# Performance work log

Hardware: AMD Instinct MI355X
Metric: run time of the kernel (lower is better)

Reference implementation:

```python
import jax, jax.numpy as jnp
import numpy as np

DIM = 1024
FF = 4096
E = 8
K = 2


def setup_inputs() -> dict:
    key = jax.random.key(0)
    ks = jax.random.split(key, 6)
    x = jax.random.normal(ks[0], (4, 2048, DIM), dtype=jnp.float32)
    wr = jax.random.normal(ks[1], (E, DIM), dtype=jnp.float32) * 0.02   # router weight [E, D]
    w1 = jax.random.normal(ks[2], (E, DIM, 2 * FF), dtype=jnp.float32) * 0.02  # SwiGLU in-proj
    b1 = jax.random.normal(ks[3], (E, 2 * FF), dtype=jnp.float32) * 0.02
    w2 = jax.random.normal(ks[4], (E, FF, DIM), dtype=jnp.float32) * 0.02  # SwiGLU out-proj
    b2 = jax.random.normal(ks[5], (E, DIM), dtype=jnp.float32) * 0.02
    return {"x": x, "wr": wr, "w1": w1, "b1": b1, "w2": w2, "b2": b2}


def reference(x, wr, w1, b1, w2, b2):
    B, T, D = x.shape
    n_experts = wr.shape[0]
    xf = x.reshape(B * T, D)                      # [N, D]
    logits = xf @ wr.T                            # [N, E]
    topk_vals, topk_idx = jax.lax.top_k(logits, K)  # [N, K]
    gates = jax.nn.softmax(topk_vals, axis=-1)      # [N, K]
    out = jnp.zeros_like(xf)
    for e in range(n_experts):
        # combined gate weight for tokens routed to expert e (0 otherwise)
        g_e = jnp.sum(jnp.where(topk_idx == e, gates, 0.0), axis=-1)  # [N]
        u = xf @ w1[e] + b1[e]                    # [N, 2F]
        a, b = jnp.split(u, 2, axis=-1)
        h = jax.nn.silu(a) * b                    # SwiGLU
        y_e = h @ w2[e] + b2[e]                   # [N, D]
        out = out + g_e[:, None] * y_e
    return out.reshape(B, T, D)
```

## Files before the change

### kernel.cpp

```cpp
#include <hip/hip_runtime.h>

#define NE 8
#define NTOK 8192
#define NDIM 1024
#define NFF 4096

typedef short bf16x8 __attribute__((ext_vector_type(8)));
typedef float f32x4 __attribute__((ext_vector_type(4)));
typedef unsigned short us_t;
typedef us_t us4 __attribute__((ext_vector_type(4)));

__device__ __forceinline__ us_t f2bf(float f) {
  unsigned int u = __float_as_uint(f);
  u += 0x7fffu + ((u >> 16) & 1u);
  return (us_t)(u >> 16);
}

__device__ __forceinline__ void gload16(const void* g, void* l) {
  __builtin_amdgcn_global_load_lds(
      (const __attribute__((address_space(1))) void*)g,
      (__attribute__((address_space(3))) void*)l, 16, 0, 0);
}

__global__ __launch_bounds__(256) void router_kernel(
    const float* __restrict__ x, const float* __restrict__ wr,
    int* __restrict__ counts, int* __restrict__ tok_list, float* __restrict__ gate_list,
    us_t* __restrict__ xbf)
{
  __shared__ float wr_s[NE * NDIM];
  int tid = threadIdx.x;
#pragma unroll
  for (int i = 0; i < 8; ++i)
    ((float4*)wr_s)[tid + 256 * i] = ((const float4*)wr)[tid + 256 * i];
  __syncthreads();
  int w = tid >> 6, l = tid & 63;
  int t = blockIdx.x * 4 + w;
  float4 xv[4];
#pragma unroll
  for (int j = 0; j < 4; ++j) xv[j] = ((const float4*)x)[(size_t)t * 256 + j * 64 + l];
#pragma unroll
  for (int j = 0; j < 4; ++j) {
    us4 o;
    o.x = f2bf(xv[j].x); o.y = f2bf(xv[j].y); o.z = f2bf(xv[j].z); o.w = f2bf(xv[j].w);
    ((us4*)xbf)[(size_t)t * 256 + j * 64 + l] = o;
  }
  float logits[NE];
#pragma unroll
  for (int e = 0; e < NE; ++e) {
    float p = 0.f;
#pragma unroll
    for (int j = 0; j < 4; ++j) {
      float4 wv = ((const float4*)wr_s)[e * 256 + j * 64 + l];
      p += xv[j].x * wv.x + xv[j].y * wv.y + xv[j].z * wv.z + xv[j].w * wv.w;
    }
#pragma unroll
    for (int s = 32; s > 0; s >>= 1) p += __shfl_xor(p, s, 64);
    logits[e] = p;
  }
  if (l == 0) {
    int e1 = 0; float v1 = logits[0];
#pragma unroll
    for (int e = 1; e < NE; ++e) if (logits[e] > v1) { v1 = logits[e]; e1 = e; }
    int e2 = -1; float v2 = -3.4e38f;
#pragma unroll
    for (int e = 0; e < NE; ++e) if (e != e1 && logits[e] > v2) { v2 = logits[e]; e2 = e; }
    float ge = expf(v2 - v1);
    float g1 = 1.f / (1.f + ge);
    float g2 = 1.f - g1;
    int i1 = atomicAdd(&counts[e1], 1);
    tok_list[e1 * NTOK + i1] = t; gate_list[e1 * NTOK + i1] = g1;
    int i2 = atomicAdd(&counts[e2], 1);
    tok_list[e2 * NTOK + i2] = t; gate_list[e2 * NTOK + i2] = g2;
  }
}

__global__ void prefix8(const int* __restrict__ counts, int* __restrict__ offsets) {
  if (threadIdx.x == 0) {
    int s = 0;
    for (int e = 0; e < NE; ++e) { offsets[e] = s; s += counts[e]; }
  }
}

__global__ __launch_bounds__(256) void transpose_cvt(
    const float* __restrict__ in, us_t* __restrict__ out, int R, int C)
{
  __shared__ float tile[64][65];
  int e = blockIdx.z;
  const float* ip = in + (size_t)e * R * C;
  us_t* op = out + (size_t)e * R * C;
  int r0 = blockIdx.y * 64, c0 = blockIdx.x * 64;
  int tid = threadIdx.x;
#pragma unroll
  for (int q = 0; q < 4; ++q) {
    int id = tid + 256 * q;
    int rr = id >> 4, c4 = id & 15;
    float4 v = *(const float4*)&ip[(size_t)(r0 + rr) * C + c0 + c4 * 4];
    tile[rr][c4 * 4 + 0] = v.x; tile[rr][c4 * 4 + 1] = v.y;
    tile[rr][c4 * 4 + 2] = v.z; tile[rr][c4 * 4 + 3] = v.w;
  }
  __syncthreads();
#pragma unroll
  for (int q = 0; q < 4; ++q) {
    int id = tid + 256 * q;
    int cc = id >> 4, r4 = id & 15;
    us4 o;
    o.x = f2bf(tile[r4 * 4 + 0][cc]);
    o.y = f2bf(tile[r4 * 4 + 1][cc]);
    o.z = f2bf(tile[r4 * 4 + 2][cc]);
    o.w = f2bf(tile[r4 * 4 + 3][cc]);
    *(us4*)&op[(size_t)(c0 + cc) * R + r0 + r4 * 4] = o;
  }
}

__global__ __launch_bounds__(256) void gemm1_swiglu(
    const us_t* __restrict__ xbf,
    const us_t* __restrict__ w1T,
    const float* __restrict__ b1,
    const int* __restrict__ counts, const int* __restrict__ offsets,
    const int* __restrict__ tok_list,
    us_t* __restrict__ hbuf)
{
  const int e = blockIdx.z, mt = blockIdx.y, ct = blockIdx.x;
  const int cnt = counts[e];
  if (mt * 128 >= cnt) return;
  const int off = offsets[e];
  const int tid = threadIdx.x, w = tid >> 6, l = tid & 63;
  const int wr_ = w >> 1, wc = w & 1;

  __shared__ char ldsA[16384];
  __shared__ char ldsB[32768];
  __shared__ int tok_l[128];

  if (tid < 128) {
    int r = mt * 128 + tid;
    tok_l[tid] = tok_list[e * NTOK + (r < cnt ? r : cnt - 1)];
  }
  __syncthreads();

  f32x4 zf = {0.f, 0.f, 0.f, 0.f};
  f32x4 acc[2][4][4];
#pragma unroll
  for (int h_ = 0; h_ < 2; ++h_)
#pragma unroll
    for (int cg = 0; cg < 4; ++cg)
#pragma unroll
      for (int rg = 0; rg < 4; ++rg) acc[h_][cg][rg] = zf;

  const size_t w1base = (size_t)e * 2 * NFF * NDIM;

  for (int kt = 0; kt < NDIM; kt += 64) {
    __syncthreads();
#pragma unroll
    for (int i = 0; i < 12; ++i) {
      int c = w + i * 4;
      const us_t* gsrc; char* ldst;
      if (c < 16) {
        int p = c * 1024 + l * 16;
        int row = p >> 7;
        int ir = (p & 127) ^ ((row & 7) << 4);
        gsrc = xbf + (size_t)tok_l[row] * NDIM + kt + (ir >> 1);
        ldst = ldsA + c * 1024;
      } else {
        int cb = c - 16;
        int p = cb * 1024 + l * 16;
        int row = p >> 7;
        int ir = (p & 127) ^ ((row & 7) << 4);
        int ncol = (row < 128) ? (ct * 128 + row) : (NFF + ct * 128 + row - 128);
        gsrc = w1T + w1base + (size_t)ncol * NDIM + kt + (ir >> 1);
        ldst = ldsB + cb * 1024;
      }
      gload16(gsrc, ldst);
    }
    __syncthreads();
#pragma unroll
    for (int ks = 0; ks < 2; ++ks) {
      bf16x8 af[4];
#pragma unroll
      for (int rg = 0; rg < 4; ++rg) {
        int row = wr_ * 64 + rg * 16 + (l & 15);
        int ir = (ks * 64 + (l >> 4) * 16) ^ ((row & 7) << 4);
        af[rg] = *(const bf16x8*)(ldsA + row * 128 + ir);
      }
#pragma unroll
      for (int h_ = 0; h_ < 2; ++h_)
#pragma unroll
        for (int cg = 0; cg < 4; ++cg) {
          int crow = h_ * 128 + wc * 64 + cg * 16 + (l & 15);
          int ir = (ks * 64 + (l >> 4) * 16) ^ ((crow & 7) << 4);
          bf16x8 bfr = *(const bf16x8*)(ldsB + crow * 128 + ir);
#pragma unroll
          for (int rg = 0; rg < 4; ++rg)
            acc[h_][cg][rg] = __builtin_amdgcn_mfma_f32_16x16x32_bf16(af[rg], bfr, acc[h_][cg][rg], 0, 0, 0);
        }
    }
  }

  float b1a[4], b1b[4];
#pragma unroll
  for (int cg = 0; cg < 4; ++cg) {
    int n_a = ct * 128 + wc * 64 + cg * 16 + (l & 15);
    b1a[cg] = b1[e * 2 * NFF + n_a];
    b1b[cg] = b1[e * 2 * NFF + NFF + n_a];
  }
#pragma unroll
  for (int cg = 0; cg < 4; ++cg) {
    int n_a = ct * 128 + wc * 64 + cg * 16 + (l & 15);
#pragma unroll
    for (int rg = 0; rg < 4; ++rg) {
#pragma unroll
      for (int j = 0; j < 4; ++j) {
        int rt = wr_ * 64 + rg * 16 + (l >> 4) * 4 + j;
        int r = mt * 128 + rt;
        if (r < cnt) {
          float a = acc[0][cg][rg][j] + b1a[cg];
          float b = acc[1][cg][rg][j] + b1b[cg];
          float hv = (a / (1.f + __expf(-a))) * b;
          hbuf[(size_t)(off + r) * NFF + n_a] = f2bf(hv);
        }
      }
    }
  }
}

__global__ __launch_bounds__(256) void gemm2_scatter(
    const us_t* __restrict__ hbuf,
    const us_t* __restrict__ w2T,
    const float* __restrict__ b2,
    const int* __restrict__ counts, const int* __restrict__ offsets,
    const int* __restrict__ tok_list, const float* __restrict__ gate_list,
    float* __restrict__ out)
{
  const int e = blockIdx.z, mt = blockIdx.y, nt = blockIdx.x;
  const int cnt = counts[e];
  if (mt * 128 >= cnt) return;
  const int off = offsets[e];
  const int tid = threadIdx.x, w = tid >> 6, l = tid & 63;
  const int wr_ = w >> 1, wc = w & 1;

  __shared__ char ldsA[16384];
  __shared__ char ldsB[16384];
  __shared__ int tok_l[128];
  __shared__ float gate_l[128];

  if (tid < 128) {
    int r = mt * 128 + tid;
    int rr = (r < cnt ? r : cnt - 1);
    tok_l[tid] = tok_list[e * NTOK + rr];
    gate_l[tid] = gate_list[e * NTOK + rr];
  }
  __syncthreads();

  f32x4 zf = {0.f, 0.f, 0.f, 0.f};
  f32x4 acc[4][4];
#pragma unroll
  for (int cg = 0; cg < 4; ++cg)
#pragma unroll
    for (int rg = 0; rg < 4; ++rg) acc[cg][rg] = zf;

  const size_t w2base = (size_t)e * NDIM * NFF;

  for (int kt = 0; kt < NFF; kt += 64) {
    __syncthreads();
#pragma unroll
    for (int i = 0; i < 8; ++i) {
      int c = w + i * 4;
      const us_t* gsrc; char* ldst;
      if (c < 16) {
        int p = c * 1024 + l * 16;
        int row = p >> 7;
        int ir = (p & 127) ^ ((row & 7) << 4);
        int r = mt * 128 + row;
        if (r >= cnt) r = cnt - 1;
        gsrc = hbuf + (size_t)(off + r) * NFF + kt + (ir >> 1);
        ldst = ldsA + c * 1024;
      } else {
        int cb = c - 16;
        int p = cb * 1024 + l * 16;
        int row = p >> 7;
        int ir = (p & 127) ^ ((row & 7) << 4);
        gsrc = w2T + w2base + (size_t)(nt * 128 + row) * NFF + kt + (ir >> 1);
        ldst = ldsB + cb * 1024;
      }
      gload16(gsrc, ldst);
    }
    __syncthreads();
#pragma unroll
    for (int ks = 0; ks < 2; ++ks) {
      bf16x8 af[4];
#pragma unroll
      for (int rg = 0; rg < 4; ++rg) {
        int row = wr_ * 64 + rg * 16 + (l & 15);
        int ir = (ks * 64 + (l >> 4) * 16) ^ ((row & 7) << 4);
        af[rg] = *(const bf16x8*)(ldsA + row * 128 + ir);
      }
#pragma unroll
      for (int cg = 0; cg < 4; ++cg) {
        int crow = wc * 64 + cg * 16 + (l & 15);
        int ir = (ks * 64 + (l >> 4) * 16) ^ ((crow & 7) << 4);
        bf16x8 bfr = *(const bf16x8*)(ldsB + crow * 128 + ir);
#pragma unroll
        for (int rg = 0; rg < 4; ++rg)
          acc[cg][rg] = __builtin_amdgcn_mfma_f32_16x16x32_bf16(af[rg], bfr, acc[cg][rg], 0, 0, 0);
      }
    }
  }

#pragma unroll
  for (int cg = 0; cg < 4; ++cg) {
    int col = nt * 128 + wc * 64 + cg * 16 + (l & 15);
    float b2v = b2[e * NDIM + col];
#pragma unroll
    for (int rg = 0; rg < 4; ++rg) {
#pragma unroll
      for (int j = 0; j < 4; ++j) {
        int rt = wr_ * 64 + rg * 16 + (l >> 4) * 4 + j;
        int r = mt * 128 + rt;
        if (r < cnt) {
          float y = acc[cg][rg][j] + b2v;
          atomicAdd(&out[(size_t)tok_l[rt] * NDIM + col], gate_l[rt] * y);
        }
      }
    }
  }
}

extern "C" void kernel_launch(void* const* d_in, const int* in_sizes, int n_in,
                              void* d_out, int out_size, void* d_ws, size_t ws_size,
                              hipStream_t stream) {
  const float* x  = (const float*)d_in[0];
  const float* wr = (const float*)d_in[1];
  const float* w1 = (const float*)d_in[2];
  const float* b1 = (const float*)d_in[3];
  const float* w2 = (const float*)d_in[4];
  const float* b2 = (const float*)d_in[5];
  float* out = (float*)d_out;
  char* ws = (char*)d_ws;

  int*   counts    = (int*)(ws + 0);
  int*   offsets   = (int*)(ws + 256);
  int*   tok_list  = (int*)(ws + 512);
  float* gate_list = (float*)(ws + 512 + NE * NTOK * 4);
  us_t*  xbf       = (us_t*)(ws + 524800);
  us_t*  hbuf      = (us_t*)(ws + 524800 + (size_t)NTOK * NDIM * 2);
  us_t*  wT        = (us_t*)(ws + 524800 + (size_t)NTOK * NDIM * 2
                                         + (size_t)2 * NTOK * NFF * 2);

  hipMemsetAsync(counts, 0, 32, stream);
  hipMemsetAsync(out, 0, (size_t)out_size * sizeof(float), stream);

  router_kernel<<<NTOK / 4, 256, 0, stream>>>(x, wr, counts, tok_list, gate_list, xbf);
  prefix8<<<1, 64, 0, stream>>>(counts, offsets);

  transpose_cvt<<<dim3(2 * NFF / 64, NDIM / 64, NE), 256, 0, stream>>>(w1, wT, NDIM, 2 * NFF);
  gemm1_swiglu<<<dim3(NFF / 128, NTOK / 128, NE), 256, 0, stream>>>(
      xbf, wT, b1, counts, offsets, tok_list, hbuf);

  transpose_cvt<<<dim3(NDIM / 64, NFF / 64, NE), 256, 0, stream>>>(w2, wT, NFF, NDIM);
  gemm2_scatter<<<dim3(NDIM / 128, NTOK / 128, NE), 256, 0, stream>>>(
      hbuf, wT, b2, counts, offsets, tok_list, gate_list, out);
}
```

Before: 1.007 ms.

## Rewrite expert GEMMs as 256x256 tiles with double-buffered LDS pipeline

Both grouped expert GEMMs move to 512-thread blocks computing 256x256 output tiles. Global-to-LDS loads are double-buffered and staged in quarters interleaved with four MFMA phases per K step, governed by explicit vmcnt/lgkmcnt waits, sched barriers and s_setprio. The aim is to hide memory latency behind MFMA work and raise data reuse per block. In exchange, LDS use rises to 128KB per block, register pressure grows, and tails are coarser for experts whose token counts are not multiples of 256.

```diff
diff --git a/kernel.cpp b/kernel.cpp
--- a/kernel.cpp
+++ b/kernel.cpp
@@ -9,6 +9,10 @@
 typedef float f32x4 __attribute__((ext_vector_type(4)));
 typedef unsigned short us_t;
 typedef us_t us4 __attribute__((ext_vector_type(4)));
+
+#define MFMA16 __builtin_amdgcn_mfma_f32_16x16x32_bf16
+#define SBAR __builtin_amdgcn_s_barrier
+#define SCHED0() __builtin_amdgcn_sched_barrier(0)
 
 __device__ __forceinline__ us_t f2bf(float f) {
   unsigned int u = __float_as_uint(f);
@@ -112,7 +116,7 @@
   }
 }
 
-__global__ __launch_bounds__(256) void gemm1_swiglu(
+__global__ __launch_bounds__(512, 2) void gemm1_swiglu(
     const us_t* __restrict__ xbf,
     const us_t* __restrict__ w1T,
     const float* __restrict__ b1,
@@ -122,107 +126,167 @@
 {
   const int e = blockIdx.z, mt = blockIdx.y, ct = blockIdx.x;
   const int cnt = counts[e];
-  if (mt * 128 >= cnt) return;
+  if (mt * 256 >= cnt) return;
   const int off = offsets[e];
   const int tid = threadIdx.x, w = tid >> 6, l = tid & 63;
-  const int wr_ = w >> 1, wc = w & 1;
-
-  __shared__ char ldsA[16384];
-  __shared__ char ldsB[32768];
-  __shared__ int tok_l[128];
-
-  if (tid < 128) {
-    int r = mt * 128 + tid;
+  const int wr_ = w >> 2, wc = w & 3;
+
+  __shared__ char ldsA[2][32768];
+  __shared__ char ldsB[2][32768];
+  __shared__ int tok_l[256];
+
+  if (tid < 256) {
+    int r = mt * 256 + tid;
     tok_l[tid] = tok_list[e * NTOK + (r < cnt ? r : cnt - 1)];
   }
   __syncthreads();
 
+  const size_t w1base = (size_t)e * (2 * NFF) * NDIM;
+
+  auto stageA = [&](char* dst, int half, int kt) {
+#pragma unroll
+    for (int q = 0; q < 2; ++q) {
+      int c = half * 16 + w * 2 + q;
+      int p = c * 1024 + l * 16;
+      int row = p >> 7;
+      int ir = (p & 127) ^ ((row & 7) << 4);
+      gload16(xbf + (size_t)tok_l[row] * NDIM + kt + (ir >> 1), dst + c * 1024);
+    }
+  };
+  auto stageB = [&](char* dst, int half, int kt) {
+#pragma unroll
+    for (int q = 0; q < 2; ++q) {
+      int c = half * 16 + w * 2 + q;
+      int p = c * 1024 + l * 16;
+      int row = p >> 7;
+      int ir = (p & 127) ^ ((row & 7) << 4);
+      int ncol = (row < 128) ? (ct * 128 + row) : (NFF + ct * 128 + (row - 128));
+      gload16(w1T + w1base + (size_t)ncol * NDIM + kt + (ir >> 1), dst + c * 1024);
+    }
+  };
+  auto readA = [&](const char* src, int mf, int ks) -> bf16x8 {
+    int row = (mf < 4 ? wr_ * 64 + mf * 16 : 128 + wr_ * 64 + (mf - 4) * 16) + (l & 15);
+    int ir = (ks * 64 + ((l >> 4) * 16)) ^ ((row & 7) << 4);
+    return *(const bf16x8*)(src + row * 128 + ir);
+  };
+  auto readB = [&](const char* src, int nf, int ks) -> bf16x8 {
+    int row = (nf < 2 ? wc * 32 + nf * 16 : 128 + wc * 32 + (nf - 2) * 16) + (l & 15);
+    int ir = (ks * 64 + ((l >> 4) * 16)) ^ ((row & 7) << 4);
+    return *(const bf16x8*)(src + row * 128 + ir);
+  };
+
+  f32x4 acc[8][4];
   f32x4 zf = {0.f, 0.f, 0.f, 0.f};
-  f32x4 acc[2][4][4];
-#pragma unroll
-  for (int h_ = 0; h_ < 2; ++h_)
-#pragma unroll
-    for (int cg = 0; cg < 4; ++cg)
-#pragma unroll
-      for (int rg = 0; rg < 4; ++rg) acc[h_][cg][rg] = zf;
-
-  const size_t w1base = (size_t)e * 2 * NFF * NDIM;
-
-  for (int kt = 0; kt < NDIM; kt += 64) {
-    __syncthreads();
-#pragma unroll
-    for (int i = 0; i < 12; ++i) {
-      int c = w + i * 4;
-      const us_t* gsrc; char* ldst;
-      if (c < 16) {
-        int p = c * 1024 + l * 16;
-        int row = p >> 7;
-        int ir = (p & 127) ^ ((row & 7) << 4);
-        gsrc = xbf + (size_t)tok_l[row] * NDIM + kt + (ir >> 1);
-        ldst = ldsA + c * 1024;
-      } else {
-        int cb = c - 16;
-        int p = cb * 1024 + l * 16;
-        int row = p >> 7;
-        int ir = (p & 127) ^ ((row & 7) << 4);
-        int ncol = (row < 128) ? (ct * 128 + row) : (NFF + ct * 128 + row - 128);
-        gsrc = w1T + w1base + (size_t)ncol * NDIM + kt + (ir >> 1);
-        ldst = ldsB + cb * 1024;
-      }
-      gload16(gsrc, ldst);
-    }
-    __syncthreads();
-#pragma unroll
-    for (int ks = 0; ks < 2; ++ks) {
-      bf16x8 af[4];
-#pragma unroll
-      for (int rg = 0; rg < 4; ++rg) {
-        int row = wr_ * 64 + rg * 16 + (l & 15);
-        int ir = (ks * 64 + (l >> 4) * 16) ^ ((row & 7) << 4);
-        af[rg] = *(const bf16x8*)(ldsA + row * 128 + ir);
-      }
-#pragma unroll
-      for (int h_ = 0; h_ < 2; ++h_)
-#pragma unroll
-        for (int cg = 0; cg < 4; ++cg) {
-          int crow = h_ * 128 + wc * 64 + cg * 16 + (l & 15);
-          int ir = (ks * 64 + (l >> 4) * 16) ^ ((crow & 7) << 4);
-          bf16x8 bfr = *(const bf16x8*)(ldsB + crow * 128 + ir);
-#pragma unroll
-          for (int rg = 0; rg < 4; ++rg)
-            acc[h_][cg][rg] = __builtin_amdgcn_mfma_f32_16x16x32_bf16(af[rg], bfr, acc[h_][cg][rg], 0, 0, 0);
-        }
-    }
-  }
-
-  float b1a[4], b1b[4];
-#pragma unroll
-  for (int cg = 0; cg < 4; ++cg) {
-    int n_a = ct * 128 + wc * 64 + cg * 16 + (l & 15);
-    b1a[cg] = b1[e * 2 * NFF + n_a];
-    b1b[cg] = b1[e * 2 * NFF + NFF + n_a];
-  }
-#pragma unroll
-  for (int cg = 0; cg < 4; ++cg) {
-    int n_a = ct * 128 + wc * 64 + cg * 16 + (l & 15);
-#pragma unroll
-    for (int rg = 0; rg < 4; ++rg) {
+#pragma unroll
+  for (int mf = 0; mf < 8; ++mf)
+#pragma unroll
+    for (int nf = 0; nf < 4; ++nf) acc[mf][nf] = zf;
+
+  const int NT = NDIM / 64;
+  stageA(ldsA[0], 0, 0); stageA(ldsA[0], 1, 0);
+  stageB(ldsB[0], 0, 0); stageB(ldsB[0], 1, 0);
+  stageB(ldsB[1], 0, 64); stageB(ldsB[1], 1, 64);
+  stageA(ldsA[1], 0, 64);
+  asm volatile("s_waitcnt vmcnt(6)" ::: "memory");
+  SCHED0();
+  SBAR();
+
+#pragma unroll 1
+  for (int t = 0; t < NT; ++t) {
+    const int b = t & 1;
+    const char* Ab = ldsA[b];
+    const char* Bb = ldsB[b];
+    bf16x8 bf_[4][2];
+    bf16x8 a0, a1, a2, a3;
+#pragma unroll
+    for (int nf = 0; nf < 4; ++nf) { bf_[nf][0] = readB(Bb, nf, 0); bf_[nf][1] = readB(Bb, nf, 1); }
+    a0 = readA(Ab, 0, 0); a1 = readA(Ab, 0, 1); a2 = readA(Ab, 1, 0); a3 = readA(Ab, 1, 1);
+    if (t + 1 < NT) stageA(ldsA[b ^ 1], 1, (t + 1) * 64);
+    SBAR();
+    asm volatile("s_waitcnt lgkmcnt(0)" ::: "memory");
+    SCHED0();
+    __builtin_amdgcn_s_setprio(1);
+#pragma unroll
+    for (int nf = 0; nf < 4; ++nf) {
+      acc[0][nf] = MFMA16(a0, bf_[nf][0], acc[0][nf], 0, 0, 0);
+      acc[0][nf] = MFMA16(a1, bf_[nf][1], acc[0][nf], 0, 0, 0);
+      acc[1][nf] = MFMA16(a2, bf_[nf][0], acc[1][nf], 0, 0, 0);
+      acc[1][nf] = MFMA16(a3, bf_[nf][1], acc[1][nf], 0, 0, 0);
+    }
+    __builtin_amdgcn_s_setprio(0);
+    SBAR();
+    a0 = readA(Ab, 2, 0); a1 = readA(Ab, 2, 1); a2 = readA(Ab, 3, 0); a3 = readA(Ab, 3, 1);
+    if (t + 2 < NT) stageB(ldsB[b], 0, (t + 2) * 64);
+    SBAR();
+    asm volatile("s_waitcnt lgkmcnt(0)" ::: "memory");
+    SCHED0();
+    __builtin_amdgcn_s_setprio(1);
+#pragma unroll
+    for (int nf = 0; nf < 4; ++nf) {
+      acc[2][nf] = MFMA16(a0, bf_[nf][0], acc[2][nf], 0, 0, 0);
+      acc[2][nf] = MFMA16(a1, bf_[nf][1], acc[2][nf], 0, 0, 0);
+      acc[3][nf] = MFMA16(a2, bf_[nf][0], acc[3][nf], 0, 0, 0);
+      acc[3][nf] = MFMA16(a3, bf_[nf][1], acc[3][nf], 0, 0, 0);
+    }
+    __builtin_amdgcn_s_setprio(0);
+    SBAR();
+    a0 = readA(Ab, 4, 0); a1 = readA(Ab, 4, 1); a2 = readA(Ab, 5, 0); a3 = readA(Ab, 5, 1);
+    if (t + 2 < NT) stageB(ldsB[b], 1, (t + 2) * 64);
+    SBAR();
+    asm volatile("s_waitcnt lgkmcnt(0)" ::: "memory");
+    SCHED0();
+    __builtin_amdgcn_s_setprio(1);
+#pragma unroll
+    for (int nf = 0; nf < 4; ++nf) {
+      acc[4][nf] = MFMA16(a0, bf_[nf][0], acc[4][nf], 0, 0, 0);
+      acc[4][nf] = MFMA16(a1, bf_[nf][1], acc[4][nf], 0, 0, 0);
+      acc[5][nf] = MFMA16(a2, bf_[nf][0], acc[5][nf], 0, 0, 0);
+      acc[5][nf] = MFMA16(a3, bf_[nf][1], acc[5][nf], 0, 0, 0);
+    }
+    __builtin_amdgcn_s_setprio(0);
+    SBAR();
+    a0 = readA(Ab, 6, 0); a1 = readA(Ab, 6, 1); a2 = readA(Ab, 7, 0); a3 = readA(Ab, 7, 1);
+    if (t + 2 < NT) stageA(ldsA[b], 0, (t + 2) * 64);
+    SBAR();
+    asm volatile("s_waitcnt lgkmcnt(0)" ::: "memory");
+    SCHED0();
+    __builtin_amdgcn_s_setprio(1);
+#pragma unroll
+    for (int nf = 0; nf < 4; ++nf) {
+      acc[6][nf] = MFMA16(a0, bf_[nf][0], acc[6][nf], 0, 0, 0);
+      acc[6][nf] = MFMA16(a1, bf_[nf][1], acc[6][nf], 0, 0, 0);
+      acc[7][nf] = MFMA16(a2, bf_[nf][0], acc[7][nf], 0, 0, 0);
+      acc[7][nf] = MFMA16(a3, bf_[nf][1], acc[7][nf], 0, 0, 0);
+    }
+    __builtin_amdgcn_s_setprio(0);
+    if (t == NT - 2) { asm volatile("s_waitcnt vmcnt(0)" ::: "memory"); SCHED0(); }
+    else if (t < NT - 2) { asm volatile("s_waitcnt vmcnt(6)" ::: "memory"); SCHED0(); }
+    SBAR();
+  }
+
+#pragma unroll
+  for (int p = 0; p < 2; ++p) {
+    int ncol = ct * 128 + wc * 32 + p * 16 + (l & 15);
+    float ba = b1[e * 2 * NFF + ncol];
+    float bb = b1[e * 2 * NFF + NFF + ncol];
+#pragma unroll
+    for (int mf = 0; mf < 8; ++mf) {
+      int rbase = (mf < 4 ? wr_ * 64 + mf * 16 : 128 + wr_ * 64 + (mf - 4) * 16) + (l >> 4) * 4;
 #pragma unroll
       for (int j = 0; j < 4; ++j) {
-        int rt = wr_ * 64 + rg * 16 + (l >> 4) * 4 + j;
-        int r = mt * 128 + rt;
+        int r = mt * 256 + rbase + j;
         if (r < cnt) {
-          float a = acc[0][cg][rg][j] + b1a[cg];
-          float b = acc[1][cg][rg][j] + b1b[cg];
-          float hv = (a / (1.f + __expf(-a))) * b;
-          hbuf[(size_t)(off + r) * NFF + n_a] = f2bf(hv);
+          float a = acc[mf][p][j] + ba;
+          float bv = acc[mf][p + 2][j] + bb;
+          float hv = (a / (1.f + __expf(-a))) * bv;
+          hbuf[(size_t)(off + r) * NFF + ncol] = f2bf(hv);
         }
       }
     }
   }
 }
 
-__global__ __launch_bounds__(256) void gemm2_scatter(
+__global__ __launch_bounds__(512, 2) void gemm2_scatter(
     const us_t* __restrict__ hbuf,
     const us_t* __restrict__ w2T,
     const float* __restrict__ b2,
@@ -232,91 +296,159 @@
 {
   const int e = blockIdx.z, mt = blockIdx.y, nt = blockIdx.x;
   const int cnt = counts[e];
-  if (mt * 128 >= cnt) return;
+  if (mt * 256 >= cnt) return;
   const int off = offsets[e];
   const int tid = threadIdx.x, w = tid >> 6, l = tid & 63;
-  const int wr_ = w >> 1, wc = w & 1;
-
-  __shared__ char ldsA[16384];
-  __shared__ char ldsB[16384];
-  __shared__ int tok_l[128];
-  __shared__ float gate_l[128];
-
-  if (tid < 128) {
-    int r = mt * 128 + tid;
+  const int wr_ = w >> 2, wc = w & 3;
+
+  __shared__ char ldsA[2][32768];
+  __shared__ char ldsB[2][32768];
+  __shared__ int tok_l[256];
+  __shared__ float gate_l[256];
+
+  if (tid < 256) {
+    int r = mt * 256 + tid;
     int rr = (r < cnt ? r : cnt - 1);
     tok_l[tid] = tok_list[e * NTOK + rr];
     gate_l[tid] = gate_list[e * NTOK + rr];
   }
   __syncthreads();
 
+  const size_t w2base = (size_t)e * NDIM * NFF;
+
+  auto stageA = [&](char* dst, int half, int kt) {
+#pragma unroll
+    for (int q = 0; q < 2; ++q) {
+      int c = half * 16 + w * 2 + q;
+      int p = c * 1024 + l * 16;
+      int row = p >> 7;
+      int ir = (p & 127) ^ ((row & 7) << 4);
+      int r = mt * 256 + row; if (r >= cnt) r = cnt - 1;
+      gload16(hbuf + (size_t)(off + r) * NFF + kt + (ir >> 1), dst + c * 1024);
+    }
+  };
+  auto stageB = [&](char* dst, int half, int kt) {
+#pragma unroll
+    for (int q = 0; q < 2; ++q) {
+      int c = half * 16 + w * 2 + q;
+      int p = c * 1024 + l * 16;
+      int row = p >> 7;
+      int ir = (p & 127) ^ ((row & 7) << 4);
+      gload16(w2T + w2base + (size_t)(nt * 256 + row) * NFF + kt + (ir >> 1), dst + c * 1024);
+    }
+  };
+  auto readA = [&](const char* src, int mf, int ks) -> bf16x8 {
+    int row = (mf < 4 ? wr_ * 64 + mf * 16 : 128 + wr_ * 64 + (mf - 4) * 16) + (l & 15);
+    int ir = (ks * 64 + ((l >> 4) * 16)) ^ ((row & 7) << 4);
+    return *(const bf16x8*)(src + row * 128 + ir);
+  };
+  auto readB = [&](const char* src, int nf, int ks) -> bf16x8 {
+    int row = wc * 64 + nf * 16 + (l & 15);
+    int ir = (ks * 64 + ((l >> 4) * 16)) ^ ((row & 7) << 4);
+    return *(const bf16x8*)(src + row * 128 + ir);
+  };
+
+  f32x4 acc[8][4];
   f32x4 zf = {0.f, 0.f, 0.f, 0.f};
-  f32x4 acc[4][4];
-#pragma unroll
-  for (int cg = 0; cg < 4; ++cg)
-#pragma unroll
-    for (int rg = 0; rg < 4; ++rg) acc[cg][rg] = zf;
-
-  const size_t w2base = (size_t)e * NDIM * NFF;
-
-  for (int kt = 0; kt < NFF; kt += 64) {
-    __syncthreads();
-#pragma unroll
-    for (int i = 0; i < 8; ++i) {
-      int c = w + i * 4;
-      const us_t* gsrc; char* ldst;
-      if (c < 16) {
-        int p = c * 1024 + l * 16;
-        int row = p >> 7;
-        int ir = (p & 127) ^ ((row & 7) << 4);
-        int r = mt * 128 + row;
-        if (r >= cnt) r = cnt - 1;
-        gsrc = hbuf + (size_t)(off + r) * NFF + kt + (ir >> 1);
-        ldst = ldsA + c * 1024;
-      } else {
-        int cb = c - 16;
-        int p = cb * 1024 + l * 16;
-        int row = p >> 7;
-        int ir = (p & 127) ^ ((row & 7) << 4);
-        gsrc = w2T + w2base + (size_t)(nt * 128 + row) * NFF + kt + (ir >> 1);
-        ldst = ldsB + cb * 1024;
-      }
-      gload16(gsrc, ldst);
-    }
-    __syncthreads();
-#pragma unroll
-    for (int ks = 0; ks < 2; ++ks) {
-      bf16x8 af[4];
-#pragma unroll
-      for (int rg = 0; rg < 4; ++rg) {
-        int row = wr_ * 64 + rg * 16 + (l & 15);
-        int ir = (ks * 64 + (l >> 4) * 16) ^ ((row & 7) << 4);
-        af[rg] = *(const bf16x8*)(ldsA + row * 128 + ir);
-      }
-#pragma unroll
-      for (int cg = 0; cg < 4; ++cg) {
-        int crow = wc * 64 + cg * 16 + (l & 15);
-        int ir = (ks * 64 + (l >> 4) * 16) ^ ((crow & 7) << 4);
-        bf16x8 bfr = *(const bf16x8*)(ldsB + crow * 128 + ir);
-#pragma unroll
-        for (int rg = 0; rg < 4; ++rg)
-          acc[cg][rg] = __builtin_amdgcn_mfma_f32_16x16x32_bf16(af[rg], bfr, acc[cg][rg], 0, 0, 0);
-      }
-    }
-  }
-
-#pragma unroll
-  for (int cg = 0; cg < 4; ++cg) {
-    int col = nt * 128 + wc * 64 + cg * 16 + (l & 15);
+#pragma unroll
+  for (int mf = 0; mf < 8; ++mf)
+#pragma unroll
+    for (int nf = 0; nf < 4; ++nf) acc[mf][nf] = zf;
+
+  const int NT = NFF / 64;
+  stageA(ldsA[0], 0, 0); stageA(ldsA[0], 1, 0);
+  stageB(ldsB[0], 0, 0); stageB(ldsB[0], 1, 0);
+  stageB(ldsB[1], 0, 64); stageB(ldsB[1], 1, 64);
+  stageA(ldsA[1], 0, 64);
+  asm volatile("s_waitcnt vmcnt(6)" ::: "memory");
+  SCHED0();
+  SBAR();
+
+#pragma unroll 1
+  for (int t = 0; t < NT; ++t) {
+    const int b = t & 1;
+    const char* Ab = ldsA[b];
+    const char* Bb = ldsB[b];
+    bf16x8 bf_[4][2];
+    bf16x8 a0, a1, a2, a3;
+#pragma unroll
+    for (int nf = 0; nf < 4; ++nf) { bf_[nf][0] = readB(Bb, nf, 0); bf_[nf][1] = readB(Bb, nf, 1); }
+    a0 = readA(Ab, 0, 0); a1 = readA(Ab, 0, 1); a2 = readA(Ab, 1, 0); a3 = readA(Ab, 1, 1);
+    if (t + 1 < NT) stageA(ldsA[b ^ 1], 1, (t + 1) * 64);
+    SBAR();
+    asm volatile("s_waitcnt lgkmcnt(0)" ::: "memory");
+    SCHED0();
+    __builtin_amdgcn_s_setprio(1);
+#pragma unroll
+    for (int nf = 0; nf < 4; ++nf) {
+      acc[0][nf] = MFMA16(a0, bf_[nf][0], acc[0][nf], 0, 0, 0);
+      acc[0][nf] = MFMA16(a1, bf_[nf][1], acc[0][nf], 0, 0, 0);
+      acc[1][nf] = MFMA16(a2, bf_[nf][0], acc[1][nf], 0, 0, 0);
+      acc[1][nf] = MFMA16(a3, bf_[nf][1], acc[1][nf], 0, 0, 0);
+    }
+    __builtin_amdgcn_s_setprio(0);
+    SBAR();
+    a0 = readA(Ab, 2, 0); a1 = readA(Ab, 2, 1); a2 = readA(Ab, 3, 0); a3 = readA(Ab, 3, 1);
+    if (t + 2 < NT) stageB(ldsB[b], 0, (t + 2) * 64);
+    SBAR();
+    asm volatile("s_waitcnt lgkmcnt(0)" ::: "memory");
+    SCHED0();
+    __builtin_amdgcn_s_setprio(1);
+#pragma unroll
+    for (int nf = 0; nf < 4; ++nf) {
+      acc[2][nf] = MFMA16(a0, bf_[nf][0], acc[2][nf], 0, 0, 0);
+      acc[2][nf] = MFMA16(a1, bf_[nf][1], acc[2][nf], 0, 0, 0);
+      acc[3][nf] = MFMA16(a2, bf_[nf][0], acc[3][nf], 0, 0, 0);
+      acc[3][nf] = MFMA16(a3, bf_[nf][1], acc[3][nf], 0, 0, 0);
+    }
+    __builtin_amdgcn_s_setprio(0);
+    SBAR();
+    a0 = readA(Ab, 4, 0); a1 = readA(Ab, 4, 1); a2 = readA(Ab, 5, 0); a3 = readA(Ab, 5, 1);
+    if (t + 2 < NT) stageB(ldsB[b], 1, (t + 2) * 64);
+    SBAR();
+    asm volatile("s_waitcnt lgkmcnt(0)" ::: "memory");
+    SCHED0();
+    __builtin_amdgcn_s_setprio(1);
+#pragma unroll
+    for (int nf = 0; nf < 4; ++nf) {
+      acc[4][nf] = MFMA16(a0, bf_[nf][0], acc[4][nf], 0, 0, 0);
+      acc[4][nf] = MFMA16(a1, bf_[nf][1], acc[4][nf], 0, 0, 0);
+      acc[5][nf] = MFMA16(a2, bf_[nf][0], acc[5][nf], 0, 0, 0);
+      acc[5][nf] = MFMA16(a3, bf_[nf][1], acc[5][nf], 0, 0, 0);
+    }
+    __builtin_amdgcn_s_setprio(0);
+    SBAR();
+    a0 = readA(Ab, 6, 0); a1 = readA(Ab, 6, 1); a2 = readA(Ab, 7, 0); a3 = readA(Ab, 7, 1);
+    if (t + 2 < NT) stageA(ldsA[b], 0, (t + 2) * 64);
+    SBAR();
+    asm volatile("s_waitcnt lgkmcnt(0)" ::: "memory");
+    SCHED0();
+    __builtin_amdgcn_s_setprio(1);
+#pragma unroll
+    for (int nf = 0; nf < 4; ++nf) {
+      acc[6][nf] = MFMA16(a0, bf_[nf][0], acc[6][nf], 0, 0, 0);
+      acc[6][nf] = MFMA16(a1, bf_[nf][1], acc[6][nf], 0, 0, 0);
+      acc[7][nf] = MFMA16(a2, bf_[nf][0], acc[7][nf], 0, 0, 0);
+      acc[7][nf] = MFMA16(a3, bf_[nf][1], acc[7][nf], 0, 0, 0);
+    }
+    __builtin_amdgcn_s_setprio(0);
+    if (t == NT - 2) { asm volatile("s_waitcnt vmcnt(0)" ::: "memory"); SCHED0(); }
+    else if (t < NT - 2) { asm volatile("s_waitcnt vmcnt(6)" ::: "memory"); SCHED0(); }
+    SBAR();
+  }
+
+#pragma unroll
+  for (int nf = 0; nf < 4; ++nf) {
+    int col = nt * 256 + wc * 64 + nf * 16 + (l & 15);
     float b2v = b2[e * NDIM + col];
 #pragma unroll
-    for (int rg = 0; rg < 4; ++rg) {
+    for (int mf = 0; mf < 8; ++mf) {
+      int rbase = (mf < 4 ? wr_ * 64 + mf * 16 : 128 + wr_ * 64 + (mf - 4) * 16) + (l >> 4) * 4;
 #pragma unroll
       for (int j = 0; j < 4; ++j) {
-        int rt = wr_ * 64 + rg * 16 + (l >> 4) * 4 + j;
-        int r = mt * 128 + rt;
-        if (r < cnt) {
-          float y = acc[cg][rg][j] + b2v;
+        int rt = rbase + j;
+        if (mt * 256 + rt < cnt) {
+          float y = acc[mf][nf][j] + b2v;
           atomicAdd(&out[(size_t)tok_l[rt] * NDIM + col], gate_l[rt] * y);
         }
       }
@@ -352,10 +484,10 @@
   prefix8<<<1, 64, 0, stream>>>(counts, offsets);
 
   transpose_cvt<<<dim3(2 * NFF / 64, NDIM / 64, NE), 256, 0, stream>>>(w1, wT, NDIM, 2 * NFF);
-  gemm1_swiglu<<<dim3(NFF / 128, NTOK / 128, NE), 256, 0, stream>>>(
+  gemm1_swiglu<<<dim3(NFF / 128, NTOK / 256, NE), 512, 0, stream>>>(
       xbf, wT, b1, counts, offsets, tok_list, hbuf);
 
   transpose_cvt<<<dim3(NDIM / 64, NFF / 64, NE), 256, 0, stream>>>(w2, wT, NFF, NDIM);
-  gemm2_scatter<<<dim3(NDIM / 128, NTOK / 128, NE), 256, 0, stream>>>(
+  gemm2_scatter<<<dim3(NDIM / 256, NTOK / 256, NE), 512, 0, stream>>>(
       hbuf, wT, b2, counts, offsets, tok_list, gate_list, out);
 }
```

New measurement: 1.060 ms. +5.3%, slower.

## Replace atomic scatter with slot-buffer output and per-token combine; precompute load offsets

Applied to the files above, without the earlier changes.

gemm2 now writes each expert's biased output rows to a dense slot buffer instead of issuing float atomicAdds into the output. A new combine kernel reads each token's two slot rows and gate weights (recorded by the router) and writes the weighted sum, which removes the output memset and atomic contention. Both GEMMs also precompute their per-thread global load byte offsets once, taking the address arithmetic and token lookups out of the K loop. In exchange there is an extra fp32 intermediate buffer of about 64 MB and one more kernel launch.

```diff
diff --git a/kernel.cpp b/kernel.cpp
--- a/kernel.cpp
+++ b/kernel.cpp
@@ -10,6 +10,8 @@
 typedef unsigned short us_t;
 typedef us_t us4 __attribute__((ext_vector_type(4)));
 
+#define MFMA16 __builtin_amdgcn_mfma_f32_16x16x32_bf16
+
 __device__ __forceinline__ us_t f2bf(float f) {
   unsigned int u = __float_as_uint(f);
   u += 0x7fffu + ((u >> 16) & 1u);
@@ -24,7 +26,8 @@
 
 __global__ __launch_bounds__(256) void router_kernel(
     const float* __restrict__ x, const float* __restrict__ wr,
-    int* __restrict__ counts, int* __restrict__ tok_list, float* __restrict__ gate_list,
+    int* __restrict__ counts, int* __restrict__ tok_list,
+    int4* __restrict__ tok4, float2* __restrict__ gate2,
     us_t* __restrict__ xbf)
 {
   __shared__ float wr_s[NE * NDIM];
@@ -68,9 +71,11 @@
     float g1 = 1.f / (1.f + ge);
     float g2 = 1.f - g1;
     int i1 = atomicAdd(&counts[e1], 1);
-    tok_list[e1 * NTOK + i1] = t; gate_list[e1 * NTOK + i1] = g1;
+    tok_list[e1 * NTOK + i1] = t;
     int i2 = atomicAdd(&counts[e2], 1);
-    tok_list[e2 * NTOK + i2] = t; gate_list[e2 * NTOK + i2] = g2;
+    tok_list[e2 * NTOK + i2] = t;
+    tok4[t] = make_int4(e1, i1, e2, i2);
+    gate2[t] = make_float2(g1, g2);
   }
 }
 
@@ -137,6 +142,25 @@
   }
   __syncthreads();
 
+  unsigned int soff[12];
+#pragma unroll
+  for (int i = 0; i < 12; ++i) {
+    int c = w + i * 4;
+    if (i < 4) {
+      int p = c * 1024 + l * 16;
+      int row = p >> 7;
+      int ir = (p & 127) ^ ((row & 7) << 4);
+      soff[i] = (unsigned int)(tok_l[row] * 2048 + ir);
+    } else {
+      int cb = c - 16;
+      int p = cb * 1024 + l * 16;
+      int row = p >> 7;
+      int ir = (p & 127) ^ ((row & 7) << 4);
+      int ncol = (row < 128) ? (ct * 128 + row) : (NFF + ct * 128 + (row - 128));
+      soff[i] = (unsigned int)(ncol * 2048 + ir);
+    }
+  }
+
   f32x4 zf = {0.f, 0.f, 0.f, 0.f};
   f32x4 acc[2][4][4];
 #pragma unroll
@@ -146,31 +170,17 @@
 #pragma unroll
       for (int rg = 0; rg < 4; ++rg) acc[h_][cg][rg] = zf;
 
-  const size_t w1base = (size_t)e * 2 * NFF * NDIM;
-
-  for (int kt = 0; kt < NDIM; kt += 64) {
+  const char* xB = (const char*)xbf;
+  const char* wB = (const char*)w1T + (size_t)e * (2 * NFF) * NDIM * 2;
+
+  for (int ktb = 0; ktb < NDIM * 2; ktb += 128) {
     __syncthreads();
 #pragma unroll
-    for (int i = 0; i < 12; ++i) {
-      int c = w + i * 4;
-      const us_t* gsrc; char* ldst;
-      if (c < 16) {
-        int p = c * 1024 + l * 16;
-        int row = p >> 7;
-        int ir = (p & 127) ^ ((row & 7) << 4);
-        gsrc = xbf + (size_t)tok_l[row] * NDIM + kt + (ir >> 1);
-        ldst = ldsA + c * 1024;
-      } else {
-        int cb = c - 16;
-        int p = cb * 1024 + l * 16;
-        int row = p >> 7;
-        int ir = (p & 127) ^ ((row & 7) << 4);
-        int ncol = (row < 128) ? (ct * 128 + row) : (NFF + ct * 128 + row - 128);
-        gsrc = w1T + w1base + (size_t)ncol * NDIM + kt + (ir >> 1);
-        ldst = ldsB + cb * 1024;
-      }
-      gload16(gsrc, ldst);
-    }
+    for (int i = 0; i < 4; ++i)
+      gload16(xB + soff[i] + ktb, ldsA + (w + i * 4) * 1024);
+#pragma unroll
+    for (int i = 4; i < 12; ++i)
+      gload16(wB + soff[i] + ktb, ldsB + (w + i * 4 - 16) * 1024);
     __syncthreads();
 #pragma unroll
     for (int ks = 0; ks < 2; ++ks) {
@@ -190,7 +200,7 @@
           bf16x8 bfr = *(const bf16x8*)(ldsB + crow * 128 + ir);
 #pragma unroll
           for (int rg = 0; rg < 4; ++rg)
-            acc[h_][cg][rg] = __builtin_amdgcn_mfma_f32_16x16x32_bf16(af[rg], bfr, acc[h_][cg][rg], 0, 0, 0);
+            acc[h_][cg][rg] = MFMA16(af[rg], bfr, acc[h_][cg][rg], 0, 0, 0);
         }
     }
   }
@@ -222,13 +232,12 @@
   }
 }
 
-__global__ __launch_bounds__(256) void gemm2_scatter(
+__global__ __launch_bounds__(256) void gemm2_slot(
     const us_t* __restrict__ hbuf,
     const us_t* __restrict__ w2T,
     const float* __restrict__ b2,
     const int* __restrict__ counts, const int* __restrict__ offsets,
-    const int* __restrict__ tok_list, const float* __restrict__ gate_list,
-    float* __restrict__ out)
+    float* __restrict__ ybuf)
 {
   const int e = blockIdx.z, mt = blockIdx.y, nt = blockIdx.x;
   const int cnt = counts[e];
@@ -239,16 +248,25 @@
 
   __shared__ char ldsA[16384];
   __shared__ char ldsB[16384];
-  __shared__ int tok_l[128];
-  __shared__ float gate_l[128];
-
-  if (tid < 128) {
-    int r = mt * 128 + tid;
-    int rr = (r < cnt ? r : cnt - 1);
-    tok_l[tid] = tok_list[e * NTOK + rr];
-    gate_l[tid] = gate_list[e * NTOK + rr];
-  }
-  __syncthreads();
+
+  unsigned int soff[8];
+#pragma unroll
+  for (int i = 0; i < 8; ++i) {
+    int c = w + i * 4;
+    if (i < 4) {
+      int p = c * 1024 + l * 16;
+      int row = p >> 7;
+      int ir = (p & 127) ^ ((row & 7) << 4);
+      int r = mt * 128 + row; if (r >= cnt) r = cnt - 1;
+      soff[i] = (unsigned int)((off + r) * (NFF * 2) + ir);
+    } else {
+      int cb = c - 16;
+      int p = cb * 1024 + l * 16;
+      int row = p >> 7;
+      int ir = (p & 127) ^ ((row & 7) << 4);
+      soff[i] = (unsigned int)((nt * 128 + row) * (NFF * 2) + ir);
+    }
+  }
 
   f32x4 zf = {0.f, 0.f, 0.f, 0.f};
   f32x4 acc[4][4];
@@ -257,32 +275,17 @@
 #pragma unroll
     for (int rg = 0; rg < 4; ++rg) acc[cg][rg] = zf;
 
-  const size_t w2base = (size_t)e * NDIM * NFF;
-
-  for (int kt = 0; kt < NFF; kt += 64) {
+  const char* hB = (const char*)hbuf;
+  const char* wB = (const char*)w2T + (size_t)e * NDIM * NFF * 2;
+
+  for (int ktb = 0; ktb < NFF * 2; ktb += 128) {
     __syncthreads();
 #pragma unroll
-    for (int i = 0; i < 8; ++i) {
-      int c = w + i * 4;
-      const us_t* gsrc; char* ldst;
-      if (c < 16) {
-        int p = c * 1024 + l * 16;
-        int row = p >> 7;
-        int ir = (p & 127) ^ ((row & 7) << 4);
-        int r = mt * 128 + row;
-        if (r >= cnt) r = cnt - 1;
-        gsrc = hbuf + (size_t)(off + r) * NFF + kt + (ir >> 1);
-        ldst = ldsA + c * 1024;
-      } else {
-        int cb = c - 16;
-        int p = cb * 1024 + l * 16;
-        int row = p >> 7;
-        int ir = (p & 127) ^ ((row & 7) << 4);
-        gsrc = w2T + w2base + (size_t)(nt * 128 + row) * NFF + kt + (ir >> 1);
-        ldst = ldsB + cb * 1024;
-      }
-      gload16(gsrc, ldst);
-    }
+    for (int i = 0; i < 4; ++i)
+      gload16(hB + soff[i] + ktb, ldsA + (w + i * 4) * 1024);
+#pragma unroll
+    for (int i = 4; i < 8; ++i)
+      gload16(wB + soff[i] + ktb, ldsB + (w + i * 4 - 16) * 1024);
     __syncthreads();
 #pragma unroll
     for (int ks = 0; ks < 2; ++ks) {
@@ -300,7 +303,7 @@
         bf16x8 bfr = *(const bf16x8*)(ldsB + crow * 128 + ir);
 #pragma unroll
         for (int rg = 0; rg < 4; ++rg)
-          acc[cg][rg] = __builtin_amdgcn_mfma_f32_16x16x32_bf16(af[rg], bfr, acc[cg][rg], 0, 0, 0);
+          acc[cg][rg] = MFMA16(af[rg], bfr, acc[cg][rg], 0, 0, 0);
       }
     }
   }
@@ -315,13 +318,33 @@
       for (int j = 0; j < 4; ++j) {
         int rt = wr_ * 64 + rg * 16 + (l >> 4) * 4 + j;
         int r = mt * 128 + rt;
-        if (r < cnt) {
-          float y = acc[cg][rg][j] + b2v;
-          atomicAdd(&out[(size_t)tok_l[rt] * NDIM + col], gate_l[rt] * y);
-        }
-      }
-    }
-  }
+        if (r < cnt)
+          ybuf[(size_t)(off + r) * NDIM + col] = acc[cg][rg][j] + b2v;
+      }
+    }
+  }
+}
+
+__global__ __launch_bounds__(256) void combine_kernel(
+    const float* __restrict__ ybuf, const int* __restrict__ offsets,
+    const int4* __restrict__ tok4, const float2* __restrict__ gate2,
+    float* __restrict__ out)
+{
+  int t = blockIdx.x;
+  int4 p = tok4[t];
+  float2 g = gate2[t];
+  int s1 = offsets[p.x] + p.y;
+  int s2 = offsets[p.z] + p.w;
+  const float4* y1 = (const float4*)(ybuf + (size_t)s1 * NDIM);
+  const float4* y2 = (const float4*)(ybuf + (size_t)s2 * NDIM);
+  float4 a = y1[threadIdx.x];
+  float4 b = y2[threadIdx.x];
+  float4 o;
+  o.x = g.x * a.x + g.y * b.x;
+  o.y = g.x * a.y + g.y * b.y;
+  o.z = g.x * a.z + g.y * b.z;
+  o.w = g.x * a.w + g.y * b.w;
+  ((float4*)(out + (size_t)t * NDIM))[threadIdx.x] = o;
 }
 
 extern "C" void kernel_launch(void* const* d_in, const int* in_sizes, int n_in,
@@ -336,19 +359,20 @@
   float* out = (float*)d_out;
   char* ws = (char*)d_ws;
 
-  int*   counts    = (int*)(ws + 0);
-  int*   offsets   = (int*)(ws + 256);
-  int*   tok_list  = (int*)(ws + 512);
-  float* gate_list = (float*)(ws + 512 + NE * NTOK * 4);
-  us_t*  xbf       = (us_t*)(ws + 524800);
-  us_t*  hbuf      = (us_t*)(ws + 524800 + (size_t)NTOK * NDIM * 2);
-  us_t*  wT        = (us_t*)(ws + 524800 + (size_t)NTOK * NDIM * 2
-                                         + (size_t)2 * NTOK * NFF * 2);
+  int*    counts   = (int*)(ws + 0);
+  int*    offsets  = (int*)(ws + 256);
+  int*    tok_list = (int*)(ws + 512);
+  int4*   tok4     = (int4*)(ws + 512 + 262144);
+  float2* gate2    = (float2*)(ws + 512 + 262144 + 131072);
+  us_t*   xbf      = (us_t*)(ws + 524800);
+  us_t*   hbuf     = (us_t*)(ws + 524800 + (size_t)NTOK * NDIM * 2);
+  us_t*   wT       = (us_t*)(ws + 524800 + (size_t)NTOK * NDIM * 2
+                                          + (size_t)2 * NTOK * NFF * 2);
+  float*  ybuf     = (float*)((char*)wT + 67108864);
 
   hipMemsetAsync(counts, 0, 32, stream);
-  hipMemsetAsync(out, 0, (size_t)out_size * sizeof(float), stream);
-
-  router_kernel<<<NTOK / 4, 256, 0, stream>>>(x, wr, counts, tok_list, gate_list, xbf);
+
+  router_kernel<<<NTOK / 4, 256, 0, stream>>>(x, wr, counts, tok_list, tok4, gate2, xbf);
   prefix8<<<1, 64, 0, stream>>>(counts, offsets);
 
   transpose_cvt<<<dim3(2 * NFF / 64, NDIM / 64, NE), 256, 0, stream>>>(w1, wT, NDIM, 2 * NFF);
@@ -356,6 +380,8 @@
       xbf, wT, b1, counts, offsets, tok_list, hbuf);
 
   transpose_cvt<<<dim3(NDIM / 64, NFF / 64, NE), 256, 0, stream>>>(w2, wT, NFF, NDIM);
-  gemm2_scatter<<<dim3(NDIM / 128, NTOK / 128, NE), 256, 0, stream>>>(
-      hbuf, wT, b2, counts, offsets, tok_list, gate_list, out);
-}
+  gemm2_slot<<<dim3(NDIM / 128, NTOK / 128, NE), 256, 0, stream>>>(
+      hbuf, wT, b2, counts, offsets, ybuf);
+
+  combine_kernel<<<NTOK, 256, 0, stream>>>(ybuf, offsets, tok4, gate2, out);
+}
```

Measured after the change: 984.4 us. -2.2%, faster.
